# Kernel optimization log

Measured on AMD Instinct MI355X. Metric: run time of the kernel, lower is better.

## Reference

```python
import jax, jax.numpy as jnp
import numpy as np

C = 256
H = 8          # num_heads
G = 8          # groupnorm groups
EPS = 1e-6     # attention eps
GN_EPS = 1e-5  # torch GroupNorm default eps


def setup_inputs() -> dict:
    key = jax.random.key(0)
    ks = jax.random.split(key, 8)
    s = 1.0 / np.sqrt(C)
    return {
        "x": jax.random.normal(ks[0], (2, C, 32, 32, 32), dtype=jnp.float32),
        "gn_gamma": jnp.ones((C,), dtype=jnp.float32),
        "gn_beta": jnp.zeros((C,), dtype=jnp.float32),
        "wq": jax.random.normal(ks[1], (C, C), dtype=jnp.float32) * s,
        "wk": jax.random.normal(ks[2], (C, C), dtype=jnp.float32) * s,
        "wv": jax.random.normal(ks[3], (C, C), dtype=jnp.float32) * s,
        "w_out": jax.random.normal(ks[4], (C, C), dtype=jnp.float32) * s,
        "b_out": jnp.zeros((C,), dtype=jnp.float32),
    }


def reference(x, gn_gamma, gn_beta, wq, wk, wv, w_out, b_out):
    B, Cc, X, Y, Z = x.shape
    N = X * Y * Z
    D = Cc // H  # head_dim

    xf = x.reshape(B, Cc, N)

    # GroupNorm over (C/G, N) per group
    xg = xf.reshape(B, G, (Cc // G) * N)
    mean = jnp.mean(xg, axis=-1, keepdims=True)
    var = jnp.var(xg, axis=-1, keepdims=True)
    xn = ((xg - mean) * jax.lax.rsqrt(var + GN_EPS)).reshape(B, Cc, N)
    xn = xn * gn_gamma[None, :, None] + gn_beta[None, :, None]

    # 1x1x1 conv projections == channel matmuls
    q = jnp.einsum('oc,bcn->bon', wq, xn).reshape(B, H, D, N)
    k = jnp.einsum('oc,bcn->bon', wk, xn).reshape(B, H, D, N)
    v = jnp.einsum('oc,bcn->bon', wv, xn).reshape(B, H, D, N)

    qm = jax.nn.elu(q) + 1.0  # [B,H,D,N]
    km = jax.nn.elu(k) + 1.0

    # context: sum_j phi(k)_j v_j^T  -> [B,H,D,D]
    context = jnp.einsum('bhdn,bhen->bhde', km, v)
    # numerator: context @ phi(q)  -> [B,H,D,N] (axis d contracts with phi(q)'s feature dim)
    numerator = jnp.einsum('bhde,bhdn->bhen', context, qm)
    # denominator per token
    k_sum = jnp.sum(km, axis=-1)  # [B,H,D]
    denom = jnp.einsum('bhdn,bhd->bhn', qm, k_sum)  # [B,H,N]

    out = numerator / (denom[:, :, None, :] + EPS)  # [B,H,D,N]
    out = out.reshape(B, Cc, N)

    out = jnp.einsum('oc,bcn->bon', w_out, out) + b_out[None, :, None]
    out = out.reshape(B, Cc, X, Y, Z)
    return out + x
```

## Files before the change

### kernel.cpp

```cpp
#include <hip/hip_runtime.h>
#include <math.h>

#define BB 2
#define CC 256
#define NHEAD 8
#define HD 32
#define NGRP 8
#define NNTOK 32768
#define ATT_EPS 1e-6f
#define GN_EPS 1e-5f

typedef __attribute__((ext_vector_type(8))) short bfrag8;
typedef __attribute__((ext_vector_type(4))) float accf4;

__device__ __forceinline__ float b2f(unsigned short u) {
    unsigned int x = ((unsigned int)u) << 16;
    return __uint_as_float(x);
}
__device__ __forceinline__ unsigned short f2b(float f) {
    unsigned int x = __float_as_uint(f);
    unsigned int r = x + 0x7fffu + ((x >> 16) & 1u);
    return (unsigned short)(r >> 16);
}
__device__ __forceinline__ void gl_lds16(const void* g, void* s) {
    __builtin_amdgcn_global_load_lds(
        (const __attribute__((address_space(1))) unsigned int*)g,
        (__attribute__((address_space(3))) unsigned int*)s, 16, 0, 0);
}

#define WS_QMT   0ull
#define WS_XNT   (WS_QMT + 8388608ull)
#define WS_WSTOLD (WS_XNT + 8650752ull)
#define WS_PART  (WS_WSTOLD + 101632ull)
#define WS_CTX2  WS_PART
#define WS_GNP2  (WS_PART + 32768ull)
#define WS_WST2  (WS_PART + 65536ull)
#define WS_BIAS  (WS_PART + 262144ull)
#define WS_GNPO  (WS_PART + 4325376ull)
#define WS_SCALE (WS_GNPO + 2048ull)
#define WS_SHIFT (WS_SCALE + 512ull)
#define WS_CTXO  (WS_SHIFT + 512ull)
#define WS_KSUM  (WS_CTXO + 16384ull)
#define WS_AMAT  (WS_KSUM + 512ull)

#define LDS_QS_OFF  17408
#define LDS_KSP_OFF 27648
#define LDS_BIAS_OFF 49152
#define LDS_QKV_TOTAL 49664

__global__ __launch_bounds__(256) void xn_gn(const float* __restrict__ x,
                                             unsigned short* __restrict__ xn_t,
                                             float* __restrict__ gnp2) {
    __shared__ unsigned short xt[64][264];
    __shared__ float ls[64];
    int b = blockIdx.y, n0 = blockIdx.x * 64, t = threadIdx.x;
    int col4 = (t & 15) * 4;
    float gs[8], gs2[8];
    #pragma unroll
    for (int g = 0; g < 8; ++g) { gs[g] = 0.f; gs2[g] = 0.f; }
    #pragma unroll
    for (int i = 0; i < 16; ++i) {
        int c = (t >> 4) + i * 16;
        const float4 v = *(const float4*)(x + (size_t)(b * CC + c) * NNTOK + n0 + col4);
        gs[i >> 1]  += v.x + v.y + v.z + v.w;
        gs2[i >> 1] += v.x * v.x + v.y * v.y + v.z * v.z + v.w * v.w;
        xt[col4 + 0][c] = f2b(v.x);
        xt[col4 + 1][c] = f2b(v.y);
        xt[col4 + 2][c] = f2b(v.z);
        xt[col4 + 3][c] = f2b(v.w);
    }
    int lane = t & 63, w = t >> 6;
    #pragma unroll
    for (int g = 0; g < 8; ++g) {
        float a = gs[g], a2 = gs2[g];
        #pragma unroll
        for (int off = 32; off; off >>= 1) {
            a  += __shfl_down(a, off);
            a2 += __shfl_down(a2, off);
        }
        if (lane == 0) { ls[w * 16 + g * 2] = a; ls[w * 16 + g * 2 + 1] = a2; }
    }
    __syncthreads();
    if (t < 16)
        gnp2[(size_t)(b * 512 + blockIdx.x) * 16 + t] =
            ls[t] + ls[16 + t] + ls[32 + t] + ls[48 + t];
    int n = t >> 2, q = t & 3;
    const char* src = (const char*)&xt[n][0] + q * 128;
    char* dst = (char*)(xn_t + ((size_t)b * NNTOK + n0 + n) * 264) + q * 128;
    #pragma unroll
    for (int i = 0; i < 8; ++i)
        *(float4*)(dst + i * 16) = *(const float4*)(src + i * 16);
}

__global__ __launch_bounds__(256) void gn_stats2(const float* __restrict__ gnp2,
                                                 const float* __restrict__ gamma,
                                                 const float* __restrict__ beta,
                                                 float* __restrict__ scale,
                                                 float* __restrict__ shift,
                                                 float* __restrict__ ctx2) {
    __shared__ float red[256];
    __shared__ float mean_l[16], rstd_l[16];
    int t = threadIdx.x;
    for (int i = t; i < 16 * 1056; i += 256) ctx2[i] = 0.f;
    int combo = t >> 3, sl = t & 7;
    int b2 = combo >> 4, idx = combo & 15;
    float a = 0.f;
    for (int k = sl; k < 512; k += 8)
        a += gnp2[(size_t)(b2 * 512 + k) * 16 + idx];
    red[t] = a;
    __syncthreads();
    if (t < 32) {
        float s = 0.f;
        #pragma unroll
        for (int j = 0; j < 8; ++j) s += red[t * 8 + j];
        red[t] = s;
    }
    __syncthreads();
    if (t < 16) {
        const float inv = 1.0f / (float)((CC / NGRP) * NNTOK);
        float m = red[t * 2] * inv;
        float var = red[t * 2 + 1] * inv - m * m;
        mean_l[t] = m;
        rstd_l[t] = rsqrtf(var + GN_EPS);
    }
    __syncthreads();
    for (int i = t; i < BB * CC; i += 256) {
        int b = i >> 8, c = i & 255;
        int g = b * 8 + (c >> 5);
        float sc = gamma[c] * rstd_l[g];
        scale[i] = sc;
        shift[i] = beta[c] - mean_l[g] * sc;
    }
}

__global__ __launch_bounds__(256) void fold_w(const float* __restrict__ wq,
                                              const float* __restrict__ wk,
                                              const float* __restrict__ wv,
                                              const float* __restrict__ scale,
                                              const float* __restrict__ shift,
                                              unsigned short* __restrict__ Wst2,
                                              float* __restrict__ bias) {
    int slice = blockIdx.x, h = blockIdx.y, b2 = blockIdx.z, t = threadIdx.x;
    __shared__ float sc_l[256], sh_l[256];
    sc_l[t] = scale[b2 * CC + t];
    sh_l[t] = shift[b2 * CC + t];
    __syncthreads();
    const float* Ws[3] = {wq, wk, wv};
    unsigned short* wdst = Wst2 + (size_t)(b2 * NHEAD + h) * 24576;
    for (int i = slice * 3072 + t; i < (slice + 1) * 3072; i += 256) {
        int e = i & 7;
        int chunk = i >> 3;
        int lane = chunk & 63;
        int kcmi = chunk >> 6;
        int mi = kcmi % 6;
        int kc = kcmi / 6;
        int lr = lane & 15, lq = lane >> 4;
        int row = mi * 16 + lr;
        int col = kc * 32 + lq * 8 + e;
        float v = Ws[row >> 5][(size_t)(h * 32 + (row & 31)) * CC + col] * sc_l[col];
        wdst[i] = f2b(v);
    }
    if (t < 96) {
        int rl = t >> 3, sub = t & 7;
        int r = slice * 12 + rl;
        const float* wrow = Ws[r >> 5] + (size_t)(h * 32 + (r & 31)) * CC + sub * 32;
        float sp = 0.f;
        #pragma unroll
        for (int k = 0; k < 8; ++k) {
            const float4 v4 = *(const float4*)(wrow + k * 4);
            const float* shp = &sh_l[sub * 32 + k * 4];
            sp += v4.x * shp[0] + v4.y * shp[1] + v4.z * shp[2] + v4.w * shp[3];
        }
        sp += __shfl_xor(sp, 1);
        sp += __shfl_xor(sp, 2);
        sp += __shfl_xor(sp, 4);
        if (sub == 0) bias[(size_t)(b2 * NHEAD + h) * 96 + r] = sp;
    }
}

__global__ __launch_bounds__(256, 3) void qkv_ctx(
    const unsigned short* __restrict__ xn_t, const unsigned short* __restrict__ Wst2,
    const float* __restrict__ bias,
    unsigned short* __restrict__ qm_t, float* __restrict__ ctx2) {
    __shared__ char lds[LDS_QKV_TOTAL];
    const int id = blockIdx.x;
    const int xcd = id & 7;
    const int j = id >> 3;
    const int h = j & 7;
    const int rem = j >> 3;
    const int tile = xcd * 32 + (rem & 31);
    const int b = rem >> 5;
    const int t = threadIdx.x;
    const int lane = t & 63, w = t >> 6;
    const int lr = lane & 15, lq = lane >> 4;
    const int n0 = tile * 128;

    {
        const char* wg = (const char*)(Wst2 + (size_t)(b * NHEAD + h) * 24576);
        for (int jj = w; jj < 48; jj += 4)
            gl_lds16(wg + jj * 1024 + lane * 16, lds + jj * 1024);
        if (t < 96)
            ((float*)(lds + LDS_BIAS_OFF))[t] = bias[(size_t)(b * NHEAD + h) * 96 + t];
    }
    __syncthreads();

    accf4 acc[6][2];
    #pragma unroll
    for (int i = 0; i < 6; ++i)
        #pragma unroll
        for (int jj = 0; jj < 2; ++jj) acc[i][jj] = (accf4){0.f, 0.f, 0.f, 0.f};

    const unsigned short* xr0 = xn_t + ((size_t)b * NNTOK + n0 + w * 32 + lr) * 264 + lq * 8;
    const unsigned short* xr1 = xr0 + 16 * 264;
    const char* wl = lds;

    bfrag8 wnx[6], bnx[2];
    #pragma unroll
    for (int mi = 0; mi < 6; ++mi)
        wnx[mi] = *(const bfrag8*)(wl + (0 * 6 + mi) * 1024 + lane * 16);
    bnx[0] = *(const bfrag8*)xr0;
    bnx[1] = *(const bfrag8*)xr1;

    #pragma unroll
    for (int kc = 0; kc < 8; ++kc) {
        bfrag8 wcur[6];
        #pragma unroll
        for (int mi = 0; mi < 6; ++mi) wcur[mi] = wnx[mi];
        bfrag8 bcur[2] = {bnx[0], bnx[1]};
        if (kc < 7) {
            #pragma unroll
            for (int mi = 0; mi < 6; ++mi)
                wnx[mi] = *(const bfrag8*)(wl + ((kc + 1) * 6 + mi) * 1024 + lane * 16);
            bnx[0] = *(const bfrag8*)(xr0 + (kc + 1) * 32);
            bnx[1] = *(const bfrag8*)(xr1 + (kc + 1) * 32);
        }
        #pragma unroll
        for (int mi = 0; mi < 6; ++mi)
            #pragma unroll
            for (int ci = 0; ci < 2; ++ci)
                acc[mi][ci] = __builtin_amdgcn_mfma_f32_16x16x32_bf16(wcur[mi], bcur[ci], acc[mi][ci], 0, 0, 0);
    }
    __syncthreads();

    const float* biasl = (const float*)(lds + LDS_BIAS_OFF);
    char* kmv = lds;
    char* qs  = lds + LDS_QS_OFF;
    #pragma unroll
    for (int mi = 0; mi < 2; ++mi)
        #pragma unroll
        for (int ci = 0; ci < 2; ++ci)
            #pragma unroll
            for (int r = 0; r < 4; ++r) {
                int d = mi * 16 + lq * 4 + r;
                int n = w * 32 + ci * 16 + lr;
                float q = acc[mi][ci][r] + biasl[d];
                *(unsigned short*)(qs + n * 80 + d * 2) = f2b(q > 0.f ? q + 1.f : __expf(q));
            }
    #pragma unroll
    for (int mi = 2; mi < 4; ++mi)
        #pragma unroll
        for (int ci = 0; ci < 2; ++ci)
            #pragma unroll
            for (int r = 0; r < 4; ++r) {
                int d = (mi - 2) * 16 + lq * 4 + r;
                int n = w * 32 + ci * 16 + lr;
                float kk = acc[mi][ci][r] + biasl[32 + d];
                *(unsigned short*)(kmv + d * 272 + n * 2) = f2b(kk > 0.f ? kk + 1.f : __expf(kk));
            }
    #pragma unroll
    for (int mi = 4; mi < 6; ++mi)
        #pragma unroll
        for (int ci = 0; ci < 2; ++ci)
            #pragma unroll
            for (int r = 0; r < 4; ++r) {
                int e = (mi - 4) * 16 + lq * 4 + r;
                int n = w * 32 + ci * 16 + lr;
                *(unsigned short*)(kmv + (32 + e) * 272 + n * 2) = f2b(acc[mi][ci][r] + biasl[64 + e]);
            }
    __syncthreads();

    float* ctx2p = ctx2 + (size_t)(b * NHEAD + h) * 1056;

    {
        char* qg = (char*)(qm_t + ((size_t)(b * NHEAD + h) * NNTOK + n0) * 32);
        int n = t >> 1, half = t & 1;
        const char* src = qs + n * 80 + half * 32;
        char* dst = qg + n * 64 + half * 32;
        *(float4*)dst = *(const float4*)src;
        *(float4*)(dst + 16) = *(const float4*)(src + 16);
    }

    {
        int qr = w >> 1, qc = w & 1;
        accf4 cacc = (accf4){0.f, 0.f, 0.f, 0.f};
        #pragma unroll
        for (int kk = 0; kk < 4; ++kk) {
            bfrag8 a  = *(const bfrag8*)(kmv + (qr * 16 + lr) * 272 + kk * 64 + lq * 16);
            bfrag8 bb = *(const bfrag8*)(kmv + (32 + qc * 16 + lr) * 272 + kk * 64 + lq * 16);
            cacc = __builtin_amdgcn_mfma_f32_16x16x32_bf16(a, bb, cacc, 0, 0, 0);
        }
        #pragma unroll
        for (int r = 0; r < 4; ++r) {
            int d = qr * 16 + lq * 4 + r, e = qc * 16 + lr;
            atomicAdd(ctx2p + d * 32 + e, cacc[r]);
        }
    }

    {
        float* ksp = (float*)(lds + LDS_KSP_OFF);
        int d = t >> 3, oc = t & 7;
        float s = 0.f;
        for (int i = 0; i < 16; ++i)
            s += b2f(*(const unsigned short*)(kmv + d * 272 + (oc * 16 + i) * 2));
        ksp[d * 8 + oc] = s;
        __syncthreads();
        if (t < 32) {
            float s2 = 0.f;
            #pragma unroll
            for (int i = 0; i < 8; ++i) s2 += ksp[t * 8 + i];
            atomicAdd(ctx2p + 1024 + t, s2);
        }
    }
}

__global__ __launch_bounds__(256) void build_A(const float* __restrict__ w_out,
                                               const float* __restrict__ ctx2,
                                               unsigned short* __restrict__ Amat,
                                               float* __restrict__ ksum_g) {
    int ot = blockIdx.x, b = blockIdx.y, t = threadIdx.x;
    __shared__ float cs[NHEAD * HD * HD];
    for (int i = t; i < NHEAD * HD * HD; i += 256) {
        int hh = i >> 10, de = i & 1023;
        cs[i] = ctx2[(size_t)(b * NHEAD + hh) * 1056 + de];
    }
    if (ot == 0)
        ksum_g[b * CC + t] = ctx2[(size_t)(b * NHEAD + (t >> 5)) * 1056 + 1024 + (t & 31)];
    __syncthreads();
    int h = t >> 5, d = t & 31;
    for (int oi = 0; oi < 32; ++oi) {
        int o = ot * 32 + oi;
        const float* wrow = w_out + (size_t)o * CC + h * HD;
        float s = 0.f;
        #pragma unroll
        for (int e = 0; e < HD; ++e) s += wrow[e] * cs[h * 1024 + d * 32 + e];
        Amat[((size_t)(b * CC + o)) * CC + t] = f2b(s);
    }
}

#define LDSF_A   0
#define LDSF_Q   10240
#define LDSF_BO  20480
#define LDSF_KS  20992
#define LDSF_TOT 22016
__global__ __launch_bounds__(256, 4) void final_out(
    const unsigned short* __restrict__ qm_t, const unsigned short* __restrict__ Amat,
    const float* __restrict__ ksum_g, const float* __restrict__ b_out,
    const float* __restrict__ x, float* __restrict__ out) {
    __shared__ char L[LDSF_TOT];
    int tile = blockIdx.x, mt = blockIdx.y, b = blockIdx.z;
    int n0 = tile * 128, t = threadIdx.x;
    int lane = t & 63, w = t >> 6, lr = lane & 15, lq = lane >> 4;
    int wm = (w >> 1) * 64, wn = (w & 1) * 64;
    accf4 acc[4][4];
    #pragma unroll
    for (int i = 0; i < 4; ++i)
        #pragma unroll
        for (int j = 0; j < 4; ++j) acc[i][j] = (accf4){0.f, 0.f, 0.f, 0.f};

    if (t < 128) ((float*)(L + LDSF_BO))[t] = b_out[mt * 128 + t];
    ((float*)(L + LDSF_KS))[t] = ksum_g[b * CC + t];

    char* Al = L + LDSF_A;
    char* Ql = L + LDSF_Q;
    const int m = t >> 1, half = t & 1;
    const char* ag = (const char*)(Amat + (size_t)(b * CC + mt * 128 + m) * CC) + half * 32;
    const char* qg = (const char*)(qm_t + ((size_t)b * NHEAD * NNTOK + (size_t)(n0 + m)) * 32) + half * 32;

    bfrag8 a0 = *(const bfrag8*)ag;
    bfrag8 a1 = *(const bfrag8*)(ag + 16);
    bfrag8 q0 = *(const bfrag8*)qg;
    bfrag8 q1 = *(const bfrag8*)(qg + 16);

    __syncthreads();

    for (int h = 0; h < NHEAD; ++h) {
        const float* ks = (const float*)(L + LDSF_KS) + h * 32 + half * 16;
        float sp = 0.f;
        #pragma unroll
        for (int e = 0; e < 8; ++e) {
            sp += b2f((unsigned short)q0[e]) * ks[e];
            sp += b2f((unsigned short)q1[e]) * ks[8 + e];
        }
        float dot = sp + __shfl_xor(sp, 1);
        float dn = 1.0f / (dot + ATT_EPS);

        __syncthreads();
        *(bfrag8*)(Al + m * 80 + half * 32) = a0;
        *(bfrag8*)(Al + m * 80 + half * 32 + 16) = a1;
        bfrag8 s0, s1;
        #pragma unroll
        for (int e = 0; e < 8; ++e) {
            s0[e] = (short)f2b(b2f((unsigned short)q0[e]) * dn);
            s1[e] = (short)f2b(b2f((unsigned short)q1[e]) * dn);
        }
        *(bfrag8*)(Ql + m * 80 + half * 32) = s0;
        *(bfrag8*)(Ql + m * 80 + half * 32 + 16) = s1;
        __syncthreads();

        if (h < 7) {
            a0 = *(const bfrag8*)(ag + (h + 1) * 64);
            a1 = *(const bfrag8*)(ag + (h + 1) * 64 + 16);
            q0 = *(const bfrag8*)(qg + (size_t)(h + 1) * NNTOK * 64);
            q1 = *(const bfrag8*)(qg + (size_t)(h + 1) * NNTOK * 64 + 16);
        }

        bfrag8 bfr[4];
        #pragma unroll
        for (int ci = 0; ci < 4; ++ci) {
            int n = wn + ci * 16 + lr;
            bfr[ci] = *(const bfrag8*)(Ql + n * 80 + lq * 16);
        }
        #pragma unroll
        for (int mi = 0; mi < 4; ++mi) {
            bfrag8 a = *(const bfrag8*)(Al + (wm + mi * 16 + lr) * 80 + lq * 16);
            #pragma unroll
            for (int ci = 0; ci < 4; ++ci)
                acc[mi][ci] = __builtin_amdgcn_mfma_f32_16x16x32_bf16(a, bfr[ci], acc[mi][ci], 0, 0, 0);
        }
    }

    const float* bo_s = (const float*)(L + LDSF_BO);
    #pragma unroll
    for (int mi = 0; mi < 4; ++mi)
        #pragma unroll
        for (int ci = 0; ci < 4; ++ci)
            #pragma unroll
            for (int r = 0; r < 4; ++r) {
                int ol = wm + mi * 16 + lq * 4 + r;
                int n = wn + ci * 16 + lr;
                size_t idx = ((size_t)(b * CC + mt * 128 + ol)) * NNTOK + n0 + n;
                out[idx] = acc[mi][ci][r] + bo_s[ol] + x[idx];
            }
}

extern "C" void kernel_launch(void* const* d_in, const int* in_sizes, int n_in,
                              void* d_out, int out_size, void* d_ws, size_t ws_size,
                              hipStream_t stream) {
    (void)in_sizes; (void)n_in; (void)out_size; (void)ws_size;
    const float* x      = (const float*)d_in[0];
    const float* gamma  = (const float*)d_in[1];
    const float* beta   = (const float*)d_in[2];
    const float* wq     = (const float*)d_in[3];
    const float* wk     = (const float*)d_in[4];
    const float* wv     = (const float*)d_in[5];
    const float* w_out  = (const float*)d_in[6];
    const float* b_out  = (const float*)d_in[7];
    float* out = (float*)d_out;
    float* ws  = (float*)d_ws;

    unsigned short* qm_t = (unsigned short*)(ws + WS_QMT);
    unsigned short* xn_t = (unsigned short*)(ws + WS_XNT);
    float* ctx2 = ws + WS_CTX2;
    float* gnp2 = ws + WS_GNP2;
    unsigned short* Wst2 = (unsigned short*)(ws + WS_WST2);
    float* bias = ws + WS_BIAS;
    float* scale = ws + WS_SCALE;
    float* shift = ws + WS_SHIFT;
    float* ksum = ws + WS_KSUM;
    unsigned short* Amat = (unsigned short*)(ws + WS_AMAT);

    hipLaunchKernelGGL(xn_gn, dim3(NNTOK / 64, BB), dim3(256), 0, stream, x, xn_t, gnp2);
    hipLaunchKernelGGL(gn_stats2, dim3(1), dim3(256), 0, stream, gnp2, gamma, beta,
                       scale, shift, ctx2);
    hipLaunchKernelGGL(fold_w, dim3(8, 8, 2), dim3(256), 0, stream, wq, wk, wv,
                       scale, shift, Wst2, bias);
    hipLaunchKernelGGL(qkv_ctx, dim3(NNTOK / 128 * NHEAD * BB), dim3(256), 0, stream,
                       xn_t, Wst2, bias, qm_t, ctx2);
    hipLaunchKernelGGL(build_A, dim3(8, BB), dim3(256), 0, stream, w_out, ctx2, Amat, ksum);
    hipLaunchKernelGGL(final_out, dim3(NNTOK / 128, 2, BB), dim3(256), 0, stream,
                       qm_t, Amat, ksum, b_out, x, out);
}
```

Measured before the change: 244.4 us.

## Vectorize xn_gn LDS transpose, spread ctx2 zeroing, prefetch all xn fragments

```diff
diff --git a/kernel.cpp b/kernel.cpp
--- a/kernel.cpp
+++ b/kernel.cpp
@@ -33,9 +33,9 @@
 #define WS_WSTOLD (WS_XNT + 8650752ull)
 #define WS_PART  (WS_WSTOLD + 101632ull)
 #define WS_CTX2  WS_PART
-#define WS_GNP2  (WS_PART + 32768ull)
-#define WS_WST2  (WS_PART + 65536ull)
-#define WS_BIAS  (WS_PART + 262144ull)
+#define WS_GNP2  (WS_PART + 135168ull)
+#define WS_WST2  (WS_PART + 151552ull)
+#define WS_BIAS  (WS_PART + 348160ull)
 #define WS_GNPO  (WS_PART + 4325376ull)
 #define WS_SCALE (WS_GNPO + 2048ull)
 #define WS_SHIFT (WS_SCALE + 512ull)
@@ -52,38 +52,43 @@
                                              unsigned short* __restrict__ xn_t,
                                              float* __restrict__ gnp2) {
     __shared__ unsigned short xt[64][264];
-    __shared__ float ls[64];
     int b = blockIdx.y, n0 = blockIdx.x * 64, t = threadIdx.x;
-    int col4 = (t & 15) * 4;
-    float gs[8], gs2[8];
-    #pragma unroll
-    for (int g = 0; g < 8; ++g) { gs[g] = 0.f; gs2[g] = 0.f; }
+    int g16 = t >> 4, ip = t & 15, col4 = ip * 4;
+    float gs = 0.f, gs2 = 0.f;
+    bfrag8 pk0, pk1, pk2, pk3;
     #pragma unroll
     for (int i = 0; i < 16; ++i) {
-        int c = (t >> 4) + i * 16;
+        int c = g16 * 16 + i;
         const float4 v = *(const float4*)(x + (size_t)(b * CC + c) * NNTOK + n0 + col4);
-        gs[i >> 1]  += v.x + v.y + v.z + v.w;
-        gs2[i >> 1] += v.x * v.x + v.y * v.y + v.z * v.z + v.w * v.w;
-        xt[col4 + 0][c] = f2b(v.x);
-        xt[col4 + 1][c] = f2b(v.y);
-        xt[col4 + 2][c] = f2b(v.z);
-        xt[col4 + 3][c] = f2b(v.w);
+        gs  += v.x + v.y + v.z + v.w;
+        gs2 += v.x * v.x + v.y * v.y + v.z * v.z + v.w * v.w;
+        int k = i & 7;
+        pk0[k] = (short)f2b(v.x);
+        pk1[k] = (short)f2b(v.y);
+        pk2[k] = (short)f2b(v.z);
+        pk3[k] = (short)f2b(v.w);
+        if (k == 7) {
+            int cb = g16 * 32 + (i >> 3) * 16;
+            char* base = (char*)&xt[0][0] + cb;
+            *(bfrag8*)(base + (col4 + 0) * 528) = pk0;
+            *(bfrag8*)(base + (col4 + 1) * 528) = pk1;
+            *(bfrag8*)(base + (col4 + 2) * 528) = pk2;
+            *(bfrag8*)(base + (col4 + 3) * 528) = pk3;
+        }
     }
     int lane = t & 63, w = t >> 6;
     #pragma unroll
-    for (int g = 0; g < 8; ++g) {
-        float a = gs[g], a2 = gs2[g];
-        #pragma unroll
-        for (int off = 32; off; off >>= 1) {
-            a  += __shfl_down(a, off);
-            a2 += __shfl_down(a2, off);
-        }
-        if (lane == 0) { ls[w * 16 + g * 2] = a; ls[w * 16 + g * 2 + 1] = a2; }
-    }
-    __syncthreads();
-    if (t < 16)
-        gnp2[(size_t)(b * 512 + blockIdx.x) * 16 + t] =
-            ls[t] + ls[16 + t] + ls[32 + t] + ls[48 + t];
+    for (int off = 16; off; off >>= 1) {
+        gs  += __shfl_down(gs, off);
+        gs2 += __shfl_down(gs2, off);
+    }
+    if (lane == 0 || lane == 32) {
+        int g = 2 * w + (lane >> 5);
+        float* gp = gnp2 + (size_t)(b * 512 + blockIdx.x) * 16;
+        gp[g * 2] = gs;
+        gp[g * 2 + 1] = gs2;
+    }
+    __syncthreads();
     int n = t >> 2, q = t & 3;
     const char* src = (const char*)&xt[n][0] + q * 128;
     char* dst = (char*)(xn_t + ((size_t)b * NNTOK + n0 + n) * 264) + q * 128;
@@ -96,12 +101,10 @@
                                                  const float* __restrict__ gamma,
                                                  const float* __restrict__ beta,
                                                  float* __restrict__ scale,
-                                                 float* __restrict__ shift,
-                                                 float* __restrict__ ctx2) {
+                                                 float* __restrict__ shift) {
     __shared__ float red[256];
     __shared__ float mean_l[16], rstd_l[16];
     int t = threadIdx.x;
-    for (int i = t; i < 16 * 1056; i += 256) ctx2[i] = 0.f;
     int combo = t >> 3, sl = t & 7;
     int b2 = combo >> 4, idx = combo & 15;
     float a = 0.f;
@@ -139,8 +142,14 @@
                                               const float* __restrict__ scale,
                                               const float* __restrict__ shift,
                                               unsigned short* __restrict__ Wst2,
-                                              float* __restrict__ bias) {
+                                              float* __restrict__ bias,
+                                              float* __restrict__ ctx2) {
     int slice = blockIdx.x, h = blockIdx.y, b2 = blockIdx.z, t = threadIdx.x;
+    {
+        int lin = slice + h * 8 + b2 * 64;
+        int i = lin * 132 + t;
+        if (t < 132) ctx2[i] = 0.f;
+    }
     __shared__ float sc_l[256], sh_l[256];
     sc_l[t] = scale[b2 * CC + t];
     sh_l[t] = shift[b2 * CC + t];
@@ -202,43 +211,44 @@
         if (t < 96)
             ((float*)(lds + LDS_BIAS_OFF))[t] = bias[(size_t)(b * NHEAD + h) * 96 + t];
     }
-    __syncthreads();
-
-    accf4 acc[6][2];
-    #pragma unroll
-    for (int i = 0; i < 6; ++i)
-        #pragma unroll
-        for (int jj = 0; jj < 2; ++jj) acc[i][jj] = (accf4){0.f, 0.f, 0.f, 0.f};
 
     const unsigned short* xr0 = xn_t + ((size_t)b * NNTOK + n0 + w * 32 + lr) * 264 + lq * 8;
     const unsigned short* xr1 = xr0 + 16 * 264;
+    bfrag8 bnx[8][2];
+    #pragma unroll
+    for (int kc = 0; kc < 8; ++kc) {
+        bnx[kc][0] = *(const bfrag8*)(xr0 + kc * 32);
+        bnx[kc][1] = *(const bfrag8*)(xr1 + kc * 32);
+    }
+    __syncthreads();
+
+    accf4 acc[6][2];
+    #pragma unroll
+    for (int i = 0; i < 6; ++i)
+        #pragma unroll
+        for (int jj = 0; jj < 2; ++jj) acc[i][jj] = (accf4){0.f, 0.f, 0.f, 0.f};
+
     const char* wl = lds;
-
-    bfrag8 wnx[6], bnx[2];
+    bfrag8 wnx[6];
     #pragma unroll
     for (int mi = 0; mi < 6; ++mi)
         wnx[mi] = *(const bfrag8*)(wl + (0 * 6 + mi) * 1024 + lane * 16);
-    bnx[0] = *(const bfrag8*)xr0;
-    bnx[1] = *(const bfrag8*)xr1;
 
     #pragma unroll
     for (int kc = 0; kc < 8; ++kc) {
         bfrag8 wcur[6];
         #pragma unroll
         for (int mi = 0; mi < 6; ++mi) wcur[mi] = wnx[mi];
-        bfrag8 bcur[2] = {bnx[0], bnx[1]};
         if (kc < 7) {
             #pragma unroll
             for (int mi = 0; mi < 6; ++mi)
                 wnx[mi] = *(const bfrag8*)(wl + ((kc + 1) * 6 + mi) * 1024 + lane * 16);
-            bnx[0] = *(const bfrag8*)(xr0 + (kc + 1) * 32);
-            bnx[1] = *(const bfrag8*)(xr1 + (kc + 1) * 32);
         }
         #pragma unroll
         for (int mi = 0; mi < 6; ++mi)
             #pragma unroll
             for (int ci = 0; ci < 2; ++ci)
-                acc[mi][ci] = __builtin_amdgcn_mfma_f32_16x16x32_bf16(wcur[mi], bcur[ci], acc[mi][ci], 0, 0, 0);
+                acc[mi][ci] = __builtin_amdgcn_mfma_f32_16x16x32_bf16(wcur[mi], bnx[kc][ci], acc[mi][ci], 0, 0, 0);
     }
     __syncthreads();
 
@@ -471,9 +481,9 @@
 
     hipLaunchKernelGGL(xn_gn, dim3(NNTOK / 64, BB), dim3(256), 0, stream, x, xn_t, gnp2);
     hipLaunchKernelGGL(gn_stats2, dim3(1), dim3(256), 0, stream, gnp2, gamma, beta,
-                       scale, shift, ctx2);
+                       scale, shift);
     hipLaunchKernelGGL(fold_w, dim3(8, 8, 2), dim3(256), 0, stream, wq, wk, wv,
-                       scale, shift, Wst2, bias);
+                       scale, shift, Wst2, bias, ctx2);
     hipLaunchKernelGGL(qkv_ctx, dim3(NNTOK / 128 * NHEAD * BB), dim3(256), 0, stream,
                        xn_t, Wst2, bias, qm_t, ctx2);
     hipLaunchKernelGGL(build_A, dim3(8, BB), dim3(256), 0, stream, w_out, ctx2, Amat, ksum);
```

Result: faster. 237.4 us (-2.9%).
